# Optimization experiments

Hardware: AMD Instinct MI355X
Metric: run time of the kernel (lower is better)

The kernel has to match this reference:

```python
import jax, jax.numpy as jnp
import numpy as np

N_HEADS = 8   # n_heads
L = 2         # num_layers (= args.upper_T_num_layers)
H = 64        # hidden_size (= args.upper_T_hidden_dim)
F = 64        # input features
T = 12        # seq_len (= args.n_his)
N = 16384     # node_num (= LSTM batch dim)


def setup_inputs() -> dict:
    key = jax.random.key(0)
    ks = jax.random.split(key, 10)
    s = 0.05
    x = jax.random.normal(ks[0], (T, N, F), jnp.float32)
    # Stacked per-head, per-layer LSTM weights (PyTorch gate order: i, f, g, o).
    # Layer 0 input dim F == H so all layers stack cleanly.
    W_ih = jax.random.normal(ks[1], (L, N_HEADS, 4 * H, H), jnp.float32) * s
    W_hh = jax.random.normal(ks[2], (L, N_HEADS, 4 * H, H), jnp.float32) * s
    b_ih = jax.random.normal(ks[3], (L, N_HEADS, 4 * H), jnp.float32) * s
    b_hh = jax.random.normal(ks[4], (L, N_HEADS, 4 * H), jnp.float32) * s
    # Learned initial states (xavier-init nn.Parameters in the original).
    h0 = jax.random.normal(ks[5], (N_HEADS, L, N, H), jnp.float32) * s
    c0 = jax.random.normal(ks[6], (N_HEADS, L, N, H), jnp.float32) * s
    # 1x1 Conv2d(n_heads*n_his -> n_his): pure channel mixing.
    conv_w = jax.random.normal(ks[7], (T, N_HEADS * T), jnp.float32) * s
    conv_b = jax.random.normal(ks[8], (T,), jnp.float32) * s
    return {"x": x, "W_ih": W_ih, "W_hh": W_hh, "b_ih": b_ih, "b_hh": b_hh,
            "h0": h0, "c0": c0, "conv_w": conv_w, "conv_b": conv_b}


def _scan_lstm(gi, Whh, bhh, h0, c0):
    # gi: (T, heads, N, 4H) precomputed input contribution; h0/c0: (heads, N, H)
    def step(carry, g_t):
        h, c = carry
        gates = g_t + jnp.einsum('and,agd->ang', h, Whh) + bhh[:, None, :]
        i, f, g, o = jnp.split(gates, 4, axis=-1)
        c = jax.nn.sigmoid(f) * c + jax.nn.sigmoid(i) * jnp.tanh(g)
        h = jax.nn.sigmoid(o) * jnp.tanh(c)
        return (h, c), h
    (_, _), hs = jax.lax.scan(step, (h0, c0), gi)
    return hs  # (T, heads, N, H)


def reference(x, W_ih, W_hh, b_ih, b_hh, h0, c0, conv_w, conv_b):
    n_layers, n_heads = W_ih.shape[0], W_ih.shape[1]
    t_len, n_nodes, _ = x.shape
    hdim = W_hh.shape[-1]
    # Layer 0: input x is shared across heads; precompute input gates outside scan.
    gi = jnp.einsum('tnd,agd->tang', x, W_ih[0]) + b_ih[0][None, :, None, :]
    hs = _scan_lstm(gi, W_hh[0], b_hh[0], h0[:, 0], c0[:, 0])
    for l in range(1, n_layers):
        gi = jnp.einsum('tand,agd->tang', hs, W_ih[l]) + b_ih[l][None, :, None, :]
        hs = _scan_lstm(gi, W_hh[l], b_hh[l], h0[:, l], c0[:, l])
    # torch.cat over heads: head-major, then time -> channel dim = heads*T
    cat = jnp.transpose(hs, (1, 0, 2, 3)).reshape(n_heads * t_len, n_nodes, hdim)
    # 1x1 conv == channel mixing over (heads*T) -> T
    out = jnp.einsum('cnh,oc->onh', cat, conv_w) + conv_b[:, None, None]
    return out[None]  # (1, T, N, H)
```

## Files before the change

kernel.cpp:

```cpp
#include <hip/hip_runtime.h>
#include <hip/hip_bf16.h>


#define T_LEN 12
#define NHEADS 8
#define HD 64
#define NNODES 16384
#define MT 16
#define LDSP 72
#define WIH_ELEMS (2 * NHEADS * 4 * HD * HD)

typedef __bf16 bf16_t;
typedef __attribute__((ext_vector_type(2))) __bf16 bf16x2;
typedef __attribute__((ext_vector_type(4))) __bf16 bf16x4;
typedef __attribute__((ext_vector_type(8))) __bf16 bf16x8;
typedef __attribute__((ext_vector_type(4))) float f32x4;

#define MFMA16(a, b, c) __builtin_amdgcn_mfma_f32_16x16x32_bf16((a), (b), (c), 0, 0, 0)

#if __has_builtin(__builtin_amdgcn_exp2f)
#define EXP2(x) __builtin_amdgcn_exp2f(x)
#else
#define EXP2(x) exp2f(x)
#endif

__device__ __forceinline__ float fast_sigmoid(float v) {
    return __builtin_amdgcn_rcpf(1.0f + __expf(-v));
}
__device__ __forceinline__ float fast_tanh(float v) {
    return 2.0f * __builtin_amdgcn_rcpf(1.0f + __expf(-2.0f * v)) - 1.0f;
}

__device__ __forceinline__ bf16x8 load8f(const float* p) {
    f32x4 a = *(const f32x4*)p;
    f32x4 b = *(const f32x4*)(p + 4);
    bf16x8 r;
    r[0] = (bf16_t)a[0]; r[1] = (bf16_t)a[1]; r[2] = (bf16_t)a[2]; r[3] = (bf16_t)a[3];
    r[4] = (bf16_t)b[0]; r[5] = (bf16_t)b[1]; r[6] = (bf16_t)b[2]; r[7] = (bf16_t)b[3];
    return r;
}
__device__ __forceinline__ bf16x4 load4f(const float* p) {
    f32x4 a = *(const f32x4*)p;
    bf16x4 r;
    r[0] = (bf16_t)a[0]; r[1] = (bf16_t)a[1]; r[2] = (bf16_t)a[2]; r[3] = (bf16_t)a[3];
    return r;
}

template<bool SC>
__device__ __forceinline__ bf16x4 lstm_pointwise_sw(const f32x4* acc, float* creg) {
    float cn[4], so[4], tc[4];
    #pragma unroll
    for (int r = 0; r < 4; ++r) {
        float ei, ef, eg, eo;
        if (SC) {
            ei = EXP2(-acc[0][r]); ef = EXP2(-acc[1][r]);
            eg = EXP2(-acc[2][r]); eo = EXP2(-acc[3][r]);
        } else {
            ei = __expf(-acc[0][r]); ef = __expf(-acc[1][r]);
            eg = __expf(-2.0f * acc[2][r]); eo = __expf(-acc[3][r]);
        }
        float di = 1.0f + ei, df = 1.0f + ef, dg = 1.0f + eg, do_ = 1.0f + eo;
        float pif = di * df, pgo = dg * do_;
        float rr  = __builtin_amdgcn_rcpf(pif * pgo);
        float rif = rr * pgo, rgo = rr * pif;
        float sig_i  = rif * df;
        float sig_f  = rif * di;
        float tanh_g = 2.0f * (rgo * do_) - 1.0f;
        so[r] = rgo * dg;
        float cnr = sig_f * creg[r] + sig_i * tanh_g;
        cn[r] = cnr;
        creg[r] = cnr;
    }
    float d0 = 1.0f + EXP2(cn[0] * -2.885390082f);
    float d1 = 1.0f + EXP2(cn[1] * -2.885390082f);
    float d2 = 1.0f + EXP2(cn[2] * -2.885390082f);
    float d3 = 1.0f + EXP2(cn[3] * -2.885390082f);
    float p01 = d0 * d1, p23 = d2 * d3;
    float rr  = __builtin_amdgcn_rcpf(p01 * p23);
    float r01 = rr * p23, r23 = rr * p01;
    tc[0] = 2.0f * (r01 * d1) - 1.0f;
    tc[1] = 2.0f * (r01 * d0) - 1.0f;
    tc[2] = 2.0f * (r23 * d3) - 1.0f;
    tc[3] = 2.0f * (r23 * d2) - 1.0f;
    bf16x4 hv;
    hv[0] = (bf16_t)(so[0] * tc[0]);
    hv[1] = (bf16_t)(so[1] * tc[1]);
    hv[2] = (bf16_t)(so[2] * tc[2]);
    hv[3] = (bf16_t)(so[3] * tc[3]);
    return hv;
}

__global__ __launch_bounds__(256) void cvt_bf16_kernel(
    const float* __restrict__ src, bf16_t* __restrict__ dst, int n8)
{
    int i = blockIdx.x * 256 + threadIdx.x;
    if (i < n8) *(bf16x8*)(dst + (size_t)i * 8) = load8f(src + (size_t)i * 8);
}

__global__ __launch_bounds__(256) void cvt_w_kernel(
    const float* __restrict__ src, bf16_t* __restrict__ dst, int n8)
{
    int i = blockIdx.x * 256 + threadIdx.x;
    if (i >= n8) return;
    int row  = (i >> 3) & 255;
    int gate = row >> 6;
    float sc = (gate == 2) ? 2.885390082f : 1.442695041f;
    const float* p = src + (size_t)i * 8;
    f32x4 a = *(const f32x4*)p;
    f32x4 b = *(const f32x4*)(p + 4);
    bf16x8 r;
    r[0] = (bf16_t)(a[0]*sc); r[1] = (bf16_t)(a[1]*sc);
    r[2] = (bf16_t)(a[2]*sc); r[3] = (bf16_t)(a[3]*sc);
    r[4] = (bf16_t)(b[0]*sc); r[5] = (bf16_t)(b[1]*sc);
    r[6] = (bf16_t)(b[2]*sc); r[7] = (bf16_t)(b[3]*sc);
    *(bf16x8*)(dst + (size_t)i * 8) = r;
}

template<bool PREP>
__global__ __launch_bounds__(512, 4) void lstm_pipe_kernel(
    const float* __restrict__ xg,
    const bf16_t* __restrict__ xbf,
    const float* __restrict__ Wih,
    const float* __restrict__ Whh,
    const bf16_t* __restrict__ wbf,
    const float* __restrict__ bih,
    const float* __restrict__ bhh,
    const float* __restrict__ h0g,
    const float* __restrict__ c0g,
    bf16_t* __restrict__ hsw)
{
    __shared__ __align__(16) bf16_t xT[T_LEN][MT][LDSP];
    __shared__ __align__(16) bf16_t h0A[2][MT][LDSP];
    __shared__ __align__(16) bf16_t h1A[2][MT][LDSP];
    __shared__ __align__(16) float  biasLds[2][4][4][16];

    const int tid  = threadIdx.x;
    const int w    = tid >> 6;
    const int lane = tid & 63;
    const int quad = lane >> 4;
    const int col  = lane & 15;
    const int lw   = w >> 2;
    const int wq   = w & 3;
    const int a    = blockIdx.x & (NHEADS - 1);
    const int nb   = (blockIdx.x >> 3) * MT;

    #pragma unroll
    for (int it = 0; it < 3; ++it) {
        int e    = (it * 512 + tid) * 8;
        int t    = e >> 10;
        int node = (e >> 6) & (MT - 1);
        int f    = e & (HD - 1);
        bf16x8 v;
        if (PREP) v = *(const bf16x8*)(xbf + ((size_t)t * NNODES + nb + node) * HD + f);
        else      v = load8f(xg + ((size_t)t * NNODES + nb + node) * HD + f);
        *(bf16x8*)&xT[t][node][f] = v;
    }
    {
        int e    = tid * 4;
        int l    = e >> 10;
        int node = (e >> 6) & (MT - 1);
        int hh   = e & (HD - 1);
        bf16x4 v = load4f(h0g + (((size_t)a * 2 + l) * NNODES + nb + node) * HD + hh);
        if (l == 0) *(bf16x4*)&h0A[0][node][hh] = v;
        else        *(bf16x4*)&h1A[1][node][hh] = v;
    }
    {
        int l   = tid >> 8;
        int r   = tid & 255;
        int wqi = r >> 6;
        int nii = (r >> 4) & 3;
        int gc  = r & 15;
        int off = (l * NHEADS + a) * 256 + nii * 64 + wqi * 16 + gc;
        float sc = PREP ? (nii == 2 ? 2.885390082f : 1.442695041f) : 1.0f;
        biasLds[l][wqi][nii][gc] = (bih[off] + bhh[off]) * sc;
    }

    bf16x8 wA[4][2], wB[4][2];
    #pragma unroll
    for (int ni = 0; ni < 4; ++ni)
        #pragma unroll
        for (int kf = 0; kf < 2; ++kf) {
            size_t off = (((size_t)lw * NHEADS + a) * 256 + (4 * ni + wq) * 16 + col) * HD
                       + kf * 32 + quad * 8;
            if (PREP) {
                wA[ni][kf] = *(const bf16x8*)(wbf + off);
                wB[ni][kf] = *(const bf16x8*)(wbf + WIH_ELEMS + off);
            } else {
                wA[ni][kf] = load8f(Wih + off);
                wB[ni][kf] = load8f(Whh + off);
            }
        }
    float creg[4];
    {
        f32x4 cv = *(const f32x4*)(c0g + (((size_t)a * 2 + lw) * NNODES + nb + col) * HD
                                   + wq * 16 + quad * 4);
        creg[0] = cv[0]; creg[1] = cv[1]; creg[2] = cv[2]; creg[3] = cv[3];
    }
    __syncthreads();

    int cur = 0;
    #pragma unroll 1
    for (int p = 0; p <= T_LEN; ++p) {
        const bool active = lw ? (p >= 1) : (p < T_LEN);
        if (active) {
            const bf16_t* P = lw ? &h0A[cur][0][0] : &xT[p][0][0];
            const bf16_t* Q = lw ? &h1A[cur][0][0] : &h0A[cur][0][0];
            bf16_t*       D = lw ? &h1A[cur ^ 1][0][0] : &h0A[cur ^ 1][0][0];
            const int ro = col * LDSP + quad * 8;
            bf16x8 a0 = *(const bf16x8*)(P + ro);
            bf16x8 b0 = *(const bf16x8*)(Q + ro);
            f32x4 acc[4];
            #pragma unroll
            for (int ni = 0; ni < 4; ++ni) {
                f32x4 z = *(const f32x4*)&biasLds[lw][wq][ni][quad * 4];
                z = MFMA16(wA[ni][0], a0, z);
                acc[ni] = MFMA16(wB[ni][0], b0, z);
            }
            bf16x8 a1 = *(const bf16x8*)(P + ro + 32);
            bf16x8 b1 = *(const bf16x8*)(Q + ro + 32);
            #pragma unroll
            for (int ni = 0; ni < 4; ++ni) {
                f32x4 z = MFMA16(wA[ni][1], a1, acc[ni]);
                acc[ni] = MFMA16(wB[ni][1], b1, z);
            }
            bf16x4 hv = lstm_pointwise_sw<PREP>(acc, creg);
            *(bf16x4*)(D + col * LDSP + wq * 16 + quad * 4) = hv;
            if (lw)
                *(bf16x4*)(hsw + ((size_t)(a * T_LEN + (p - 1)) * NNODES + nb + col) * HD
                           + wq * 16 + quad * 4) = hv;
        }
        __syncthreads();
        cur ^= 1;
    }
}

__global__ __launch_bounds__(256) void conv_reduce_kernel(
    const bf16_t* __restrict__ hsw,
    const float* __restrict__ cwg,
    const float* __restrict__ cbg,
    float* __restrict__ outg)
{
    int flat = blockIdx.x * 256 + threadIdx.x;
    int n  = flat >> 4;
    int h4 = (flat & 15) * 4;
    f32x4 acc[T_LEN];
    #pragma unroll
    for (int o = 0; o < T_LEN; ++o) {
        float b = cbg[o];
        acc[o][0] = b; acc[o][1] = b; acc[o][2] = b; acc[o][3] = b;
    }
    const bf16_t* src = hsw + (size_t)n * HD + h4;
    #pragma unroll 6
    for (int c = 0; c < NHEADS * T_LEN; ++c) {
        bf16x4 hv = *(const bf16x4*)(src + (size_t)c * NNODES * HD);
        float h0 = (float)hv[0], h1 = (float)hv[1], h2 = (float)hv[2], h3 = (float)hv[3];
        #pragma unroll
        for (int o = 0; o < T_LEN; ++o) {
            float cv = cwg[o * (NHEADS * T_LEN) + c];
            acc[o][0] += cv * h0; acc[o][1] += cv * h1;
            acc[o][2] += cv * h2; acc[o][3] += cv * h3;
        }
    }
    #pragma unroll
    for (int o = 0; o < T_LEN; ++o)
        *(f32x4*)(outg + ((size_t)o * NNODES + n) * HD + h4) = acc[o];
}

struct SmemT {
    __align__(16) bf16_t xT[T_LEN][MT][LDSP];
    __align__(16) bf16_t hA[2][2][MT][LDSP];
    __align__(16) float  cwf[T_LEN][NHEADS * T_LEN];
    __align__(16) float  cbf[T_LEN];
};

__global__ __launch_bounds__(256) void lstm_mono_kernel(
    const float* __restrict__ xg, const float* __restrict__ Wih,
    const float* __restrict__ Whh, const float* __restrict__ bih,
    const float* __restrict__ bhh, const float* __restrict__ h0g,
    const float* __restrict__ c0g, const float* __restrict__ cwg,
    const float* __restrict__ cbg, float* __restrict__ outg)
{
    __shared__ SmemT s;
    const int tid  = threadIdx.x;
    const int w    = tid >> 6;
    const int lane = tid & 63;
    const int quad = lane >> 4;
    const int col  = lane & 15;
    const int nb   = blockIdx.x * MT;

    #pragma unroll
    for (int it = 0; it < 6; ++it) {
        int ci   = it * 256 + tid;
        int e    = ci * 8;
        int t    = e >> 10;
        int node = (e >> 6) & (MT - 1);
        int f    = e & (HD - 1);
        *(bf16x8*)&s.xT[t][node][f] =
            load8f(xg + ((size_t)t * NNODES + nb + node) * HD + f);
    }
    for (int i = tid; i < T_LEN * NHEADS * T_LEN; i += 256)
        s.cwf[i / 96][i % 96] = cwg[i];
    if (tid < T_LEN) s.cbf[tid] = cbg[tid];

    float conv_acc[T_LEN][4];
    #pragma unroll
    for (int o = 0; o < T_LEN; ++o)
        #pragma unroll
        for (int r = 0; r < 4; ++r) conv_acc[o][r] = 0.0f;

    #pragma unroll 1
    for (int a = 0; a < NHEADS; ++a) {
        bf16x8 wih[2][4][2], whh[2][4][2];
        #pragma unroll
        for (int l = 0; l < 2; ++l)
            #pragma unroll
            for (int ni = 0; ni < 4; ++ni)
                #pragma unroll
                for (int kf = 0; kf < 2; ++kf) {
                    size_t off = (((size_t)l * NHEADS + a) * 256 + (4 * ni + w) * 16 + col) * HD
                               + kf * 32 + quad * 8;
                    wih[l][ni][kf] = load8f(Wih + off);
                    whh[l][ni][kf] = load8f(Whh + off);
                }
        float bias[2][4];
        #pragma unroll
        for (int l = 0; l < 2; ++l)
            #pragma unroll
            for (int ni = 0; ni < 4; ++ni) {
                int off = (l * NHEADS + a) * 256 + ni * 64 + w * 16 + col;
                bias[l][ni] = bih[off] + bhh[off];
            }
        float creg[2][4];
        #pragma unroll
        for (int l = 0; l < 2; ++l)
            #pragma unroll
            for (int r = 0; r < 4; ++r)
                creg[l][r] = c0g[(((size_t)a * 2 + l) * NNODES + nb + quad * 4 + r) * HD
                                 + w * 16 + col];
        {
            int e    = tid * 8;
            int l    = e >> 10;
            int node = (e >> 6) & (MT - 1);
            int hh   = e & (HD - 1);
            *(bf16x8*)&s.hA[l][0][node][hh] =
                load8f(h0g + (((size_t)a * 2 + l) * NNODES + nb + node) * HD + hh);
        }
        __syncthreads();

        int cur = 0;
        #pragma unroll 1
        for (int t = 0; t < T_LEN; ++t) {
            bf16x8 xa0 = *(const bf16x8*)&s.xT[t][col][quad * 8];
            bf16x8 xa1 = *(const bf16x8*)&s.xT[t][col][32 + quad * 8];
            bf16x8 ha0 = *(const bf16x8*)&s.hA[0][cur][col][quad * 8];
            bf16x8 ha1 = *(const bf16x8*)&s.hA[0][cur][col][32 + quad * 8];
            f32x4 acc[4];
            #pragma unroll
            for (int ni = 0; ni < 4; ++ni) {
                f32x4 z = {0.f, 0.f, 0.f, 0.f};
                z = MFMA16(xa0, wih[0][ni][0], z);
                z = MFMA16(xa1, wih[0][ni][1], z);
                z = MFMA16(ha0, whh[0][ni][0], z);
                z = MFMA16(ha1, whh[0][ni][1], z);
                acc[ni] = z;
            }
            #pragma unroll
            for (int r = 0; r < 4; ++r) {
                float ig = fast_sigmoid(acc[0][r] + bias[0][0]);
                float fg = fast_sigmoid(acc[1][r] + bias[0][1]);
                float gg = fast_tanh   (acc[2][r] + bias[0][2]);
                float og = fast_sigmoid(acc[3][r] + bias[0][3]);
                float cn = fg * creg[0][r] + ig * gg;
                creg[0][r] = cn;
                s.hA[0][cur ^ 1][quad * 4 + r][w * 16 + col] = (bf16_t)(og * fast_tanh(cn));
            }
            __syncthreads();
            bf16x8 pa0 = *(const bf16x8*)&s.hA[0][cur ^ 1][col][quad * 8];
            bf16x8 pa1 = *(const bf16x8*)&s.hA[0][cur ^ 1][col][32 + quad * 8];
            bf16x8 qa0 = *(const bf16x8*)&s.hA[1][cur][col][quad * 8];
            bf16x8 qa1 = *(const bf16x8*)&s.hA[1][cur][col][32 + quad * 8];
            #pragma unroll
            for (int ni = 0; ni < 4; ++ni) {
                f32x4 z = {0.f, 0.f, 0.f, 0.f};
                z = MFMA16(pa0, wih[1][ni][0], z);
                z = MFMA16(pa1, wih[1][ni][1], z);
                z = MFMA16(qa0, whh[1][ni][0], z);
                z = MFMA16(qa1, whh[1][ni][1], z);
                acc[ni] = z;
            }
            float hn[4];
            #pragma unroll
            for (int r = 0; r < 4; ++r) {
                float ig = fast_sigmoid(acc[0][r] + bias[1][0]);
                float fg = fast_sigmoid(acc[1][r] + bias[1][1]);
                float gg = fast_tanh   (acc[2][r] + bias[1][2]);
                float og = fast_sigmoid(acc[3][r] + bias[1][3]);
                float cn = fg * creg[1][r] + ig * gg;
                creg[1][r] = cn;
                hn[r] = og * fast_tanh(cn);
                s.hA[1][cur ^ 1][quad * 4 + r][w * 16 + col] = (bf16_t)hn[r];
            }
            #pragma unroll
            for (int o = 0; o < T_LEN; ++o) {
                float cv = s.cwf[o][a * T_LEN + t];
                #pragma unroll
                for (int r = 0; r < 4; ++r) conv_acc[o][r] += cv * hn[r];
            }
            __syncthreads();
            cur ^= 1;
        }
    }
    #pragma unroll
    for (int o = 0; o < T_LEN; ++o)
        #pragma unroll
        for (int r = 0; r < 4; ++r)
            outg[((size_t)o * NNODES + nb + quad * 4 + r) * HD + w * 16 + col] =
                conv_acc[o][r] + s.cbf[o];
}

extern "C" void kernel_launch(void* const* d_in, const int* in_sizes, int n_in,
                              void* d_out, int out_size, void* d_ws, size_t ws_size,
                              hipStream_t stream) {
    (void)in_sizes; (void)n_in; (void)out_size;
    const float* x   = (const float*)d_in[0];
    const float* Wih = (const float*)d_in[1];
    const float* Whh = (const float*)d_in[2];
    const float* bih = (const float*)d_in[3];
    const float* bhh = (const float*)d_in[4];
    const float* h0  = (const float*)d_in[5];
    const float* c0  = (const float*)d_in[6];
    const float* cw  = (const float*)d_in[7];
    const float* cb  = (const float*)d_in[8];
    const size_t hs_bytes = (size_t)NHEADS * T_LEN * NNODES * HD * sizeof(bf16_t);
    const size_t x_bytes  = (size_t)T_LEN * NNODES * HD * sizeof(bf16_t);
    const size_t w_bytes  = (size_t)2 * WIH_ELEMS * sizeof(bf16_t);
    if (ws_size >= hs_bytes + x_bytes + w_bytes) {
        bf16_t* hs  = (bf16_t*)d_ws;
        bf16_t* xbf = (bf16_t*)((char*)d_ws + hs_bytes);
        bf16_t* wbf = (bf16_t*)((char*)d_ws + hs_bytes + x_bytes);
        const int n8x = T_LEN * NNODES * HD / 8;
        const int n8w = WIH_ELEMS / 8;
        cvt_bf16_kernel<<<dim3(n8x / 256), dim3(256), 0, stream>>>(x, xbf, n8x);
        cvt_w_kernel<<<dim3((n8w + 255) / 256), dim3(256), 0, stream>>>(Wih, wbf, n8w);
        cvt_w_kernel<<<dim3((n8w + 255) / 256), dim3(256), 0, stream>>>(Whh, wbf + WIH_ELEMS, n8w);
        lstm_pipe_kernel<true><<<dim3((NNODES / MT) * NHEADS), dim3(512), 0, stream>>>(
            x, xbf, Wih, Whh, wbf, bih, bhh, h0, c0, hs);
        conv_reduce_kernel<<<dim3(NNODES * 16 / 256), dim3(256), 0, stream>>>(
            hs, cw, cb, (float*)d_out);
    } else if (ws_size >= hs_bytes) {
        bf16_t* hs = (bf16_t*)d_ws;
        lstm_pipe_kernel<false><<<dim3((NNODES / MT) * NHEADS), dim3(512), 0, stream>>>(
            x, nullptr, Wih, Whh, nullptr, bih, bhh, h0, c0, hs);
        conv_reduce_kernel<<<dim3(NNODES * 16 / 256), dim3(256), 0, stream>>>(
            hs, cw, cb, (float*)d_out);
    } else {
        lstm_mono_kernel<<<dim3(NNODES / MT), dim3(256), 0, stream>>>(
            x, Wih, Whh, bih, bhh, h0, c0, cw, cb, (float*)d_out);
    }
}
```

Before: 533.7 us.

## Process 32 nodes per block and stream x from global per timestep

Each block of the pipelined two-layer LSTM kernel now handles 32 nodes instead of 16, so the register-resident weight fragments are reused across two MFMA node tiles per step and the grid is halved. The per-block LDS copy of all 12 timesteps of x is removed; layer-0 waves instead load their x fragments straight from global memory each step. The pointwise gate math is rewritten in vector form, and launch bounds drop from 4 to 3 waves per SIMD to make room for the larger register footprint. The risk is lower occupancy and global-load latency sitting on the recurrent critical path.

Measured after the change: 578.2 us. 8.3% more time.

```diff
diff --git a/kernel.cpp b/kernel.cpp
--- a/kernel.cpp
+++ b/kernel.cpp
@@ -7,6 +7,7 @@
 #define HD 64
 #define NNODES 16384
 #define MT 16
+#define MTP 32
 #define LDSP 72
 #define WIH_ELEMS (2 * NHEADS * 4 * HD * HD)
 
@@ -39,54 +40,47 @@
     r[4] = (bf16_t)b[0]; r[5] = (bf16_t)b[1]; r[6] = (bf16_t)b[2]; r[7] = (bf16_t)b[3];
     return r;
 }
-__device__ __forceinline__ bf16x4 load4f(const float* p) {
-    f32x4 a = *(const f32x4*)p;
-    bf16x4 r;
-    r[0] = (bf16_t)a[0]; r[1] = (bf16_t)a[1]; r[2] = (bf16_t)a[2]; r[3] = (bf16_t)a[3];
-    return r;
-}
 
 template<bool SC>
-__device__ __forceinline__ bf16x4 lstm_pointwise_sw(const f32x4* acc, float* creg) {
-    float cn[4], so[4], tc[4];
+__device__ __forceinline__ bf16x4 lstm_pointwise_v(const f32x4* acc, f32x4& creg) {
+    f32x4 e_i, e_f, e_g, e_o;
     #pragma unroll
     for (int r = 0; r < 4; ++r) {
-        float ei, ef, eg, eo;
         if (SC) {
-            ei = EXP2(-acc[0][r]); ef = EXP2(-acc[1][r]);
-            eg = EXP2(-acc[2][r]); eo = EXP2(-acc[3][r]);
+            e_i[r] = EXP2(-acc[0][r]); e_f[r] = EXP2(-acc[1][r]);
+            e_g[r] = EXP2(-acc[2][r]); e_o[r] = EXP2(-acc[3][r]);
         } else {
-            ei = __expf(-acc[0][r]); ef = __expf(-acc[1][r]);
-            eg = __expf(-2.0f * acc[2][r]); eo = __expf(-acc[3][r]);
+            e_i[r] = __expf(-acc[0][r]); e_f[r] = __expf(-acc[1][r]);
+            e_g[r] = __expf(-2.0f * acc[2][r]); e_o[r] = __expf(-acc[3][r]);
         }
-        float di = 1.0f + ei, df = 1.0f + ef, dg = 1.0f + eg, do_ = 1.0f + eo;
-        float pif = di * df, pgo = dg * do_;
-        float rr  = __builtin_amdgcn_rcpf(pif * pgo);
-        float rif = rr * pgo, rgo = rr * pif;
-        float sig_i  = rif * df;
-        float sig_f  = rif * di;
-        float tanh_g = 2.0f * (rgo * do_) - 1.0f;
-        so[r] = rgo * dg;
-        float cnr = sig_f * creg[r] + sig_i * tanh_g;
-        cn[r] = cnr;
-        creg[r] = cnr;
-    }
-    float d0 = 1.0f + EXP2(cn[0] * -2.885390082f);
-    float d1 = 1.0f + EXP2(cn[1] * -2.885390082f);
-    float d2 = 1.0f + EXP2(cn[2] * -2.885390082f);
-    float d3 = 1.0f + EXP2(cn[3] * -2.885390082f);
-    float p01 = d0 * d1, p23 = d2 * d3;
-    float rr  = __builtin_amdgcn_rcpf(p01 * p23);
-    float r01 = rr * p23, r23 = rr * p01;
-    tc[0] = 2.0f * (r01 * d1) - 1.0f;
-    tc[1] = 2.0f * (r01 * d0) - 1.0f;
-    tc[2] = 2.0f * (r23 * d3) - 1.0f;
-    tc[3] = 2.0f * (r23 * d2) - 1.0f;
+    }
+    f32x4 d_i = e_i + 1.0f, d_f = e_f + 1.0f, d_g = e_g + 1.0f, d_o = e_o + 1.0f;
+    f32x4 pif = d_i * d_f, pgo = d_g * d_o, pr = pif * pgo;
+    f32x4 rr;
+    #pragma unroll
+    for (int r = 0; r < 4; ++r) rr[r] = __builtin_amdgcn_rcpf(pr[r]);
+    f32x4 rif = rr * pgo, rgo = rr * pif;
+    f32x4 s_i = rif * d_f, s_f = rif * d_i;
+    f32x4 t_g = 2.0f * (rgo * d_o) - 1.0f;
+    f32x4 s_o = rgo * d_g;
+    f32x4 cn = s_f * creg + s_i * t_g;
+    creg = cn;
+    f32x4 ec;
+    #pragma unroll
+    for (int r = 0; r < 4; ++r) ec[r] = EXP2(cn[r] * -2.885390082f);
+    f32x4 dc = ec + 1.0f;
+    float p01 = dc[0] * dc[1], p23 = dc[2] * dc[3];
+    float r2  = __builtin_amdgcn_rcpf(p01 * p23);
+    float q01 = r2 * p23, q23 = r2 * p01;
+    f32x4 tc;
+    tc[0] = 2.0f * (q01 * dc[1]) - 1.0f;
+    tc[1] = 2.0f * (q01 * dc[0]) - 1.0f;
+    tc[2] = 2.0f * (q23 * dc[3]) - 1.0f;
+    tc[3] = 2.0f * (q23 * dc[2]) - 1.0f;
+    f32x4 h = s_o * tc;
     bf16x4 hv;
-    hv[0] = (bf16_t)(so[0] * tc[0]);
-    hv[1] = (bf16_t)(so[1] * tc[1]);
-    hv[2] = (bf16_t)(so[2] * tc[2]);
-    hv[3] = (bf16_t)(so[3] * tc[3]);
+    hv[0] = (bf16_t)h[0]; hv[1] = (bf16_t)h[1];
+    hv[2] = (bf16_t)h[2]; hv[3] = (bf16_t)h[3];
     return hv;
 }
 
@@ -117,7 +111,7 @@
 }
 
 template<bool PREP>
-__global__ __launch_bounds__(512, 4) void lstm_pipe_kernel(
+__global__ __launch_bounds__(512, 3) void lstm_pipe_kernel(
     const float* __restrict__ xg,
     const bf16_t* __restrict__ xbf,
     const float* __restrict__ Wih,
@@ -129,9 +123,8 @@
     const float* __restrict__ c0g,
     bf16_t* __restrict__ hsw)
 {
-    __shared__ __align__(16) bf16_t xT[T_LEN][MT][LDSP];
-    __shared__ __align__(16) bf16_t h0A[2][MT][LDSP];
-    __shared__ __align__(16) bf16_t h1A[2][MT][LDSP];
+    __shared__ __align__(16) bf16_t h0A[2][MTP][LDSP];
+    __shared__ __align__(16) bf16_t h1A[2][MTP][LDSP];
     __shared__ __align__(16) float  biasLds[2][4][4][16];
 
     const int tid  = threadIdx.x;
@@ -142,27 +135,16 @@
     const int lw   = w >> 2;
     const int wq   = w & 3;
     const int a    = blockIdx.x & (NHEADS - 1);
-    const int nb   = (blockIdx.x >> 3) * MT;
-
-    #pragma unroll
-    for (int it = 0; it < 3; ++it) {
-        int e    = (it * 512 + tid) * 8;
-        int t    = e >> 10;
-        int node = (e >> 6) & (MT - 1);
-        int f    = e & (HD - 1);
-        bf16x8 v;
-        if (PREP) v = *(const bf16x8*)(xbf + ((size_t)t * NNODES + nb + node) * HD + f);
-        else      v = load8f(xg + ((size_t)t * NNODES + nb + node) * HD + f);
-        *(bf16x8*)&xT[t][node][f] = v;
-    }
+    const int nb   = (blockIdx.x >> 3) * MTP;
+
     {
-        int e    = tid * 4;
-        int l    = e >> 10;
-        int node = (e >> 6) & (MT - 1);
+        int e    = tid * 8;
+        int l    = e >> 11;
+        int node = (e >> 6) & (MTP - 1);
         int hh   = e & (HD - 1);
-        bf16x4 v = load4f(h0g + (((size_t)a * 2 + l) * NNODES + nb + node) * HD + hh);
-        if (l == 0) *(bf16x4*)&h0A[0][node][hh] = v;
-        else        *(bf16x4*)&h1A[1][node][hh] = v;
+        bf16x8 v = load8f(h0g + (((size_t)a * 2 + l) * NNODES + nb + node) * HD + hh);
+        if (l == 0) *(bf16x8*)&h0A[0][node][hh] = v;
+        else        *(bf16x8*)&h1A[1][node][hh] = v;
     }
     {
         int l   = tid >> 8;
@@ -190,44 +172,105 @@
                 wB[ni][kf] = load8f(Whh + off);
             }
         }
-    float creg[4];
+    f32x4 cr0, cr1;
     {
-        f32x4 cv = *(const f32x4*)(c0g + (((size_t)a * 2 + lw) * NNODES + nb + col) * HD
-                                   + wq * 16 + quad * 4);
-        creg[0] = cv[0]; creg[1] = cv[1]; creg[2] = cv[2]; creg[3] = cv[3];
+        const float* cb = c0g + (((size_t)a * 2 + lw) * NNODES + nb) * HD
+                        + wq * 16 + quad * 4;
+        cr0 = *(const f32x4*)(cb + (size_t)col * HD);
+        cr1 = *(const f32x4*)(cb + (size_t)(col + 16) * HD);
     }
     __syncthreads();
 
     int cur = 0;
     #pragma unroll 1
     for (int p = 0; p <= T_LEN; ++p) {
-        const bool active = lw ? (p >= 1) : (p < T_LEN);
-        if (active) {
-            const bf16_t* P = lw ? &h0A[cur][0][0] : &xT[p][0][0];
-            const bf16_t* Q = lw ? &h1A[cur][0][0] : &h0A[cur][0][0];
-            bf16_t*       D = lw ? &h1A[cur ^ 1][0][0] : &h0A[cur ^ 1][0][0];
-            const int ro = col * LDSP + quad * 8;
-            bf16x8 a0 = *(const bf16x8*)(P + ro);
-            bf16x8 b0 = *(const bf16x8*)(Q + ro);
-            f32x4 acc[4];
-            #pragma unroll
-            for (int ni = 0; ni < 4; ++ni) {
-                f32x4 z = *(const f32x4*)&biasLds[lw][wq][ni][quad * 4];
-                z = MFMA16(wA[ni][0], a0, z);
-                acc[ni] = MFMA16(wB[ni][0], b0, z);
-            }
-            bf16x8 a1 = *(const bf16x8*)(P + ro + 32);
-            bf16x8 b1 = *(const bf16x8*)(Q + ro + 32);
-            #pragma unroll
-            for (int ni = 0; ni < 4; ++ni) {
-                f32x4 z = MFMA16(wA[ni][1], a1, acc[ni]);
-                acc[ni] = MFMA16(wB[ni][1], b1, z);
-            }
-            bf16x4 hv = lstm_pointwise_sw<PREP>(acc, creg);
-            *(bf16x4*)(D + col * LDSP + wq * 16 + quad * 4) = hv;
-            if (lw)
-                *(bf16x4*)(hsw + ((size_t)(a * T_LEN + (p - 1)) * NNODES + nb + col) * HD
-                           + wq * 16 + quad * 4) = hv;
+        if (lw == 0) {
+            if (p < T_LEN) {
+                bf16x8 x00, x01, x10, x11;
+                if (PREP) {
+                    const bf16_t* xr = xbf + ((size_t)p * NNODES + nb) * HD + quad * 8;
+                    x00 = *(const bf16x8*)(xr + (size_t)col * HD);
+                    x01 = *(const bf16x8*)(xr + (size_t)col * HD + 32);
+                    x10 = *(const bf16x8*)(xr + (size_t)(col + 16) * HD);
+                    x11 = *(const bf16x8*)(xr + (size_t)(col + 16) * HD + 32);
+                } else {
+                    const float* xr = xg + ((size_t)p * NNODES + nb) * HD + quad * 8;
+                    x00 = load8f(xr + (size_t)col * HD);
+                    x01 = load8f(xr + (size_t)col * HD + 32);
+                    x10 = load8f(xr + (size_t)(col + 16) * HD);
+                    x11 = load8f(xr + (size_t)(col + 16) * HD + 32);
+                }
+                const bf16_t* H = &h0A[cur][0][0];
+                const int r0 = col * LDSP + quad * 8;
+                const int r1 = (col + 16) * LDSP + quad * 8;
+                bf16x8 h00 = *(const bf16x8*)(H + r0);
+                bf16x8 h01 = *(const bf16x8*)(H + r0 + 32);
+                bf16x8 h10 = *(const bf16x8*)(H + r1);
+                bf16x8 h11 = *(const bf16x8*)(H + r1 + 32);
+                f32x4 acc0[4], acc1[4];
+                #pragma unroll
+                for (int ni = 0; ni < 4; ++ni) {
+                    f32x4 z = *(const f32x4*)&biasLds[0][wq][ni][quad * 4];
+                    z = MFMA16(wB[ni][0], h00, z);
+                    z = MFMA16(wB[ni][1], h01, z);
+                    z = MFMA16(wA[ni][0], x00, z);
+                    acc0[ni] = MFMA16(wA[ni][1], x01, z);
+                }
+                #pragma unroll
+                for (int ni = 0; ni < 4; ++ni) {
+                    f32x4 z = *(const f32x4*)&biasLds[0][wq][ni][quad * 4];
+                    z = MFMA16(wB[ni][0], h10, z);
+                    z = MFMA16(wB[ni][1], h11, z);
+                    z = MFMA16(wA[ni][0], x10, z);
+                    acc1[ni] = MFMA16(wA[ni][1], x11, z);
+                }
+                bf16_t* D = &h0A[cur ^ 1][0][0];
+                bf16x4 hv0 = lstm_pointwise_v<PREP>(acc0, cr0);
+                *(bf16x4*)(D + col * LDSP + wq * 16 + quad * 4) = hv0;
+                bf16x4 hv1 = lstm_pointwise_v<PREP>(acc1, cr1);
+                *(bf16x4*)(D + (col + 16) * LDSP + wq * 16 + quad * 4) = hv1;
+            }
+        } else {
+            if (p >= 1) {
+                const bf16_t* P = &h0A[cur][0][0];
+                const bf16_t* Q = &h1A[cur][0][0];
+                const int r0 = col * LDSP + quad * 8;
+                const int r1 = (col + 16) * LDSP + quad * 8;
+                bf16x8 p00 = *(const bf16x8*)(P + r0);
+                bf16x8 p01 = *(const bf16x8*)(P + r0 + 32);
+                bf16x8 q00 = *(const bf16x8*)(Q + r0);
+                bf16x8 q01 = *(const bf16x8*)(Q + r0 + 32);
+                bf16x8 p10 = *(const bf16x8*)(P + r1);
+                bf16x8 p11 = *(const bf16x8*)(P + r1 + 32);
+                bf16x8 q10 = *(const bf16x8*)(Q + r1);
+                bf16x8 q11 = *(const bf16x8*)(Q + r1 + 32);
+                f32x4 acc0[4], acc1[4];
+                #pragma unroll
+                for (int ni = 0; ni < 4; ++ni) {
+                    f32x4 z = *(const f32x4*)&biasLds[1][wq][ni][quad * 4];
+                    z = MFMA16(wA[ni][0], p00, z);
+                    z = MFMA16(wA[ni][1], p01, z);
+                    z = MFMA16(wB[ni][0], q00, z);
+                    acc0[ni] = MFMA16(wB[ni][1], q01, z);
+                }
+                #pragma unroll
+                for (int ni = 0; ni < 4; ++ni) {
+                    f32x4 z = *(const f32x4*)&biasLds[1][wq][ni][quad * 4];
+                    z = MFMA16(wA[ni][0], p10, z);
+                    z = MFMA16(wA[ni][1], p11, z);
+                    z = MFMA16(wB[ni][0], q10, z);
+                    acc1[ni] = MFMA16(wB[ni][1], q11, z);
+                }
+                bf16_t* D = &h1A[cur ^ 1][0][0];
+                bf16_t* hb = hsw + ((size_t)(a * T_LEN + (p - 1)) * NNODES + nb) * HD
+                           + wq * 16 + quad * 4;
+                bf16x4 hv0 = lstm_pointwise_v<PREP>(acc0, cr0);
+                *(bf16x4*)(D + col * LDSP + wq * 16 + quad * 4) = hv0;
+                *(bf16x4*)(hb + (size_t)col * HD) = hv0;
+                bf16x4 hv1 = lstm_pointwise_v<PREP>(acc1, cr1);
+                *(bf16x4*)(D + (col + 16) * LDSP + wq * 16 + quad * 4) = hv1;
+                *(bf16x4*)(hb + (size_t)(col + 16) * HD) = hv1;
+            }
         }
         __syncthreads();
         cur ^= 1;
@@ -443,13 +486,13 @@
         cvt_bf16_kernel<<<dim3(n8x / 256), dim3(256), 0, stream>>>(x, xbf, n8x);
         cvt_w_kernel<<<dim3((n8w + 255) / 256), dim3(256), 0, stream>>>(Wih, wbf, n8w);
         cvt_w_kernel<<<dim3((n8w + 255) / 256), dim3(256), 0, stream>>>(Whh, wbf + WIH_ELEMS, n8w);
-        lstm_pipe_kernel<true><<<dim3((NNODES / MT) * NHEADS), dim3(512), 0, stream>>>(
+        lstm_pipe_kernel<true><<<dim3((NNODES / MTP) * NHEADS), dim3(512), 0, stream>>>(
             x, xbf, Wih, Whh, wbf, bih, bhh, h0, c0, hs);
         conv_reduce_kernel<<<dim3(NNODES * 16 / 256), dim3(256), 0, stream>>>(
             hs, cw, cb, (float*)d_out);
     } else if (ws_size >= hs_bytes) {
         bf16_t* hs = (bf16_t*)d_ws;
-        lstm_pipe_kernel<false><<<dim3((NNODES / MT) * NHEADS), dim3(512), 0, stream>>>(
+        lstm_pipe_kernel<false><<<dim3((NNODES / MTP) * NHEADS), dim3(512), 0, stream>>>(
             x, nullptr, Wih, Whh, nullptr, bih, bhh, h0, c0, hs);
         conv_reduce_kernel<<<dim3(NNODES * 16 / 256), dim3(256), 0, stream>>>(
             hs, cw, cb, (float*)d_out);
```
